# Kernel tuning notes

Measured on AMD Instinct MI355X. Metric: run time of the kernel, lower is better.

The kernel has to match this reference:

```python
import jax, jax.numpy as jnp
import numpy as np

B, N, C = 64, 196, 768
H = 12
HD = C // H            # 64
TOPK = int(0.25 * HD)  # 16
HIDDEN = int(C * 4.0)  # 3072
SCALE = HD ** -0.5
EPS = 1e-5


def layernorm(x, g, b):
    mu = jnp.mean(x, axis=-1, keepdims=True)
    var = jnp.var(x, axis=-1, keepdims=True)
    return (x - mu) * jax.lax.rsqrt(var + EPS) * g + b


def setup_inputs() -> dict:
    key = jax.random.key(0)
    ks = jax.random.split(key, 8)
    s = 0.02
    return {
        "x": jax.random.normal(ks[0], (B, N, C), jnp.float32),
        "norm1_g": jnp.ones((C,), jnp.float32),
        "norm1_b": jnp.zeros((C,), jnp.float32),
        "qk_w": jax.random.normal(ks[1], (2 * C, C), jnp.float32) * s,   # torch Linear [out,in], no bias
        "attn_proj_w": jax.random.normal(ks[2], (C, H * TOPK), jnp.float32) * s,
        "attn_proj_b": jnp.zeros((C,), jnp.float32),
        "norm2_g": jnp.ones((C,), jnp.float32),
        "norm2_b": jnp.zeros((C,), jnp.float32),
        "fc1_w": jax.random.normal(ks[3], (HIDDEN, C), jnp.float32) * s,
        "fc1_b": jnp.zeros((HIDDEN,), jnp.float32),
        "fc2_w": jax.random.normal(ks[4], (C, HIDDEN), jnp.float32) * s,
        "fc2_b": jnp.zeros((C,), jnp.float32),
    }


def reference(x, norm1_g, norm1_b, qk_w, attn_proj_w, attn_proj_b,
              norm2_g, norm2_b, fc1_w, fc1_b, fc2_w, fc2_b):
    # --- HomoAttention branch ---
    h = layernorm(x, norm1_g, norm1_b)                       # [B,N,C]
    qk = h @ qk_w.T                                          # [B,N,2C]
    qk = qk.reshape(B, N, 2, H, HD).transpose(2, 0, 3, 1, 4) # [2,B,H,N,HD]
    q, k = qk[0] * SCALE, qk[1]
    attn = jnp.einsum('bhnd,bhmd->bhnm', q, k)               # [B,H,N,N]
    top_vals, _ = jax.lax.top_k(attn, TOPK)                  # [B,H,N,TOPK]
    a = jax.nn.softmax(top_vals, axis=-1)
    a = a.transpose(0, 2, 1, 3).reshape(B, N, H * TOPK)      # [B,N,H*TOPK]
    x = x + a @ attn_proj_w.T + attn_proj_b

    # --- MLP branch ---
    h2 = layernorm(x, norm2_g, norm2_b)
    h2 = jax.nn.gelu(h2 @ fc1_w.T + fc1_b, approximate=False)
    x = x + h2 @ fc2_w.T + fc2_b
    return x
```

## Files before the change

### kernel.cpp

```cpp
#include <hip/hip_runtime.h>


#define BATCH 64
#define SEQ   196
#define CH    768
#define NHEAD 12
#define HDIM  64
#define TOPK  16
#define HID   3072
#define MROWS 12544
#define MHALF 6272
#define SCALE_F 0.125f
#define NEGBIG -3e38f

typedef __bf16 bf16x8 __attribute__((ext_vector_type(8)));
typedef float  f32x4  __attribute__((ext_vector_type(4)));

__device__ __forceinline__ unsigned short f2b(float f) {
    union { float f; unsigned int i; } c; c.f = f;
    unsigned int u = c.i;
    return (unsigned short)((u + 0x7fffu + ((u >> 16) & 1u)) >> 16);
}

__device__ __forceinline__ void async16(const unsigned short* g, unsigned short* l) {
    __builtin_amdgcn_global_load_lds(
        (const __attribute__((address_space(1))) unsigned int*)(g),
        (__attribute__((address_space(3))) unsigned int*)(l), 16, 0, 0);
}

__global__ __launch_bounds__(256) void f2b4_k(const float* __restrict__ s0, unsigned short* __restrict__ d0, int n0,
                                              const float* __restrict__ s1, unsigned short* __restrict__ d1, int n1,
                                              const float* __restrict__ s2, unsigned short* __restrict__ d2, int n2,
                                              const float* __restrict__ s3, unsigned short* __restrict__ d3, int n3)
{
    int idx = (blockIdx.x * 256 + threadIdx.x) * 4;
    const float* s; unsigned short* d; int n;
    if (idx < n0) { s = s0; d = d0; n = n0; }
    else {
        idx -= n0;
        if (idx < n1) { s = s1; d = d1; n = n1; }
        else {
            idx -= n1;
            if (idx < n2) { s = s2; d = d2; n = n2; }
            else { idx -= n2; s = s3; d = d3; n = n3; }
        }
    }
    if (idx < n) {
        float4 v = *(const float4*)(s + idx);
        ushort4 o;
        o.x = f2b(v.x); o.y = f2b(v.y); o.z = f2b(v.z); o.w = f2b(v.w);
        *(ushort4*)(d + idx) = o;
    }
}

__global__ __launch_bounds__(256) void ln_k(const float* __restrict__ x,
                                            const float* __restrict__ gw,
                                            const float* __restrict__ bw,
                                            unsigned short* __restrict__ out)
{
    const int row = blockIdx.x;
    const int tid = threadIdx.x;
    const float* xr = x + (size_t)row * CH;
    float v0 = xr[tid], v1 = xr[tid + 256], v2 = xr[tid + 512];
    float s  = v0 + v1 + v2;
    float sq = v0*v0 + v1*v1 + v2*v2;
#pragma unroll
    for (int off = 32; off > 0; off >>= 1) {
        s  += __shfl_down(s, off, 64);
        sq += __shfl_down(sq, off, 64);
    }
    __shared__ __align__(16) float red[8];
    if ((tid & 63) == 0) { red[(tid >> 6) * 2] = s; red[(tid >> 6) * 2 + 1] = sq; }
    __syncthreads();
    s  = red[0] + red[2] + red[4] + red[6];
    sq = red[1] + red[3] + red[5] + red[7];
    float mu  = s * (1.0f / CH);
    float var = sq * (1.0f / CH) - mu * mu;
    float rs  = rsqrtf(var + 1e-5f);
    unsigned short* orow = out + (size_t)row * CH;
    orow[tid]       = f2b((v0 - mu) * rs * gw[tid]       + bw[tid]);
    orow[tid + 256] = f2b((v1 - mu) * rs * gw[tid + 256] + bw[tid + 256]);
    orow[tid + 512] = f2b((v2 - mu) * rs * gw[tid + 512] + bw[tid + 512]);
}

template<int TM, int TN, bool BIAS, bool RES, bool GELU, bool OUTF>
__global__ __launch_bounds__(256, 4)
void gemm_bt(const unsigned short* __restrict__ A,
             const unsigned short* __restrict__ Bw,
             const float* __restrict__ bias,
             const float* __restrict__ resid,
             void* __restrict__ Cout,
             int M, int N, int K)
{
    constexpr int WROWS = (TM == 128) ? 2 : 1;
    constexpr int WCOLS = 4 / WROWS;
    constexpr int JF = TN / (16 * WCOLS);
    __shared__ __align__(16) unsigned short As[2][TM * 32];
    __shared__ __align__(16) unsigned short Bs[2][TN * 32];
    const int tid  = threadIdx.x;
    const int w    = tid >> 6;
    const int lane = tid & 63;

    const int gridN = gridDim.x, gridM = gridDim.y;
    const int lid = blockIdx.y * gridN + blockIdx.x;
    const int SG = 8 * gridN;
    const int sg = lid / SG, r = lid % SG;
    const int remM = gridM - sg * 8;
    int mloc, nloc;
    if (remM >= 8) { mloc = sg * 8 + (r & 7); nloc = r >> 3; }
    else           { mloc = sg * 8 + r % remM; nloc = r / remM; }
    const int tileM = mloc * TM;
    const int tileN = nloc * TN;

    const int wm = (w / WCOLS) * 64;
    const int wn = (w % WCOLS) * (JF * 16);
    const int q   = lane >> 4;
    const int l16 = lane & 15;
    const int csw = (q ^ (l16 & 3)) * 8;

    f32x4 acc[4][JF];
#pragma unroll
    for (int i = 0; i < 4; ++i)
#pragma unroll
        for (int j = 0; j < JF; ++j) acc[i][j] = (f32x4){0.f, 0.f, 0.f, 0.f};

    const int r0 = tid >> 2;
    const int g0 = ((tid & 3) ^ (r0 & 3)) * 8;

    const int kIters = K >> 5;

    auto stage = [&](int kt, int buf) {
        const size_t koff = (size_t)kt * 32 + g0;
#pragma unroll
        for (int c = 0; c < TN / 64; ++c)
            async16(Bw + (size_t)(tileN + r0 + c * 64) * K + koff,
                    &Bs[buf][(size_t)(c * 256 + w * 64) * 8]);
#pragma unroll
        for (int c = 0; c < TM / 64; ++c)
            async16(A + (size_t)(tileM + r0 + c * 64) * K + koff,
                    &As[buf][(size_t)(c * 256 + w * 64) * 8]);
    };

    stage(0, 0);
    int cur = 0;
    for (int kt = 0; kt < kIters; ++kt) {
        __syncthreads();
        if (kt + 1 < kIters) stage(kt + 1, cur ^ 1);
        bf16x8 af[4], bfr[JF];
#pragma unroll
        for (int i = 0; i < 4; ++i)
            af[i] = *(const bf16x8*)&As[cur][(wm + i * 16 + l16) * 32 + csw];
#pragma unroll
        for (int j = 0; j < JF; ++j)
            bfr[j] = *(const bf16x8*)&Bs[cur][(wn + j * 16 + l16) * 32 + csw];
#pragma unroll
        for (int i = 0; i < 4; ++i)
#pragma unroll
            for (int j = 0; j < JF; ++j)
                acc[i][j] = __builtin_amdgcn_mfma_f32_16x16x32_bf16(af[i], bfr[j], acc[i][j], 0, 0, 0);
        cur ^= 1;
    }

#pragma unroll
    for (int i = 0; i < 4; ++i) {
#pragma unroll
        for (int r2 = 0; r2 < 4; ++r2) {
            int row = tileM + wm + i * 16 + q * 4 + r2;
#pragma unroll
            for (int j = 0; j < JF; ++j) {
                int col = tileN + wn + j * 16 + l16;
                float v = acc[i][j][r2];
                if (BIAS) v += bias[col];
                if (GELU) v = 0.5f * v * (1.0f + erff(v * 0.70710678118f));
                if (RES)  v += resid[(size_t)row * N + col];
                if (OUTF) ((float*)Cout)[(size_t)row * N + col] = v;
                else      ((unsigned short*)Cout)[(size_t)row * N + col] = f2b(v);
            }
        }
    }
}

__global__ __launch_bounds__(256) void attn_topk(const unsigned short* __restrict__ qk,
                                                 unsigned short* __restrict__ aout)
{
    const int bh = blockIdx.x;
    const int b = bh / NHEAD, h = bh % NHEAD;
    __shared__ __align__(16) unsigned short Qs[208 * 64];
    __shared__ __align__(16) unsigned short Ks[208 * 64];
    const int tid = threadIdx.x;

    for (int i = tid; i < 208 * 8; i += 256) {
        int row = i >> 3, c = i & 7;
        uint4 vq = make_uint4(0, 0, 0, 0), vk = vq;
        if (row < SEQ) {
            const uint4* gp = (const uint4*)(qk + ((size_t)(b * SEQ + row) * 1536 + h * 64));
            vq = gp[c];
            vk = gp[c + 96];
        }
        int slot = c ^ (row & 7);
        *(uint4*)&Qs[row * 64 + slot * 8] = vq;
        *(uint4*)&Ks[row * 64 + slot * 8] = vk;
    }
    __syncthreads();

    const int w = tid >> 6, lane = tid & 63;
    const int q = lane >> 4, l16 = lane & 15;

    for (int tn = w; tn < 13; tn += 4) {
        const int nrow = tn * 16 + l16;
        const int nsw = nrow & 7;
        bf16x8 bq0 = *(const bf16x8*)&Qs[nrow * 64 + ((0 * 4 + q) ^ nsw) * 8];
        bf16x8 bq1 = *(const bf16x8*)&Qs[nrow * 64 + ((1 * 4 + q) ^ nsw) * 8];

        float t[TOPK];
#pragma unroll
        for (int j = 0; j < TOPK; ++j) t[j] = NEGBIG;

        for (int tm = 0; tm < 12; ++tm) {
            const int mrow = tm * 16 + l16;
            const int msw = mrow & 7;
            bf16x8 ak0 = *(const bf16x8*)&Ks[mrow * 64 + ((0 * 4 + q) ^ msw) * 8];
            bf16x8 ak1 = *(const bf16x8*)&Ks[mrow * 64 + ((1 * 4 + q) ^ msw) * 8];
            f32x4 acc = (f32x4){0.f, 0.f, 0.f, 0.f};
            acc = __builtin_amdgcn_mfma_f32_16x16x32_bf16(ak0, bq0, acc, 0, 0, 0);
            acc = __builtin_amdgcn_mfma_f32_16x16x32_bf16(ak1, bq1, acc, 0, 0, 0);
#pragma unroll
            for (int r = 0; r < 4; ++r) {
                float v = acc[r];
#pragma unroll
                for (int j = 0; j < TOPK; ++j) {
                    float mx = fmaxf(t[j], v);
                    v = fminf(t[j], v);
                    t[j] = mx;
                }
            }
        }
        {
            const int mrow = 12 * 16 + l16;
            const int msw = mrow & 7;
            bf16x8 ak0 = *(const bf16x8*)&Ks[mrow * 64 + ((0 * 4 + q) ^ msw) * 8];
            bf16x8 ak1 = *(const bf16x8*)&Ks[mrow * 64 + ((1 * 4 + q) ^ msw) * 8];
            f32x4 acc = (f32x4){0.f, 0.f, 0.f, 0.f};
            acc = __builtin_amdgcn_mfma_f32_16x16x32_bf16(ak0, bq0, acc, 0, 0, 0);
            acc = __builtin_amdgcn_mfma_f32_16x16x32_bf16(ak1, bq1, acc, 0, 0, 0);
#pragma unroll
            for (int r = 0; r < 4; ++r) {
                float v = (q == 0) ? acc[r] : NEGBIG;
#pragma unroll
                for (int j = 0; j < TOPK; ++j) {
                    float mx = fmaxf(t[j], v);
                    v = fminf(t[j], v);
                    t[j] = mx;
                }
            }
        }

#pragma unroll
        for (int stage = 0; stage < 2; ++stage) {
            const int xm = 16 << stage;
            float bl[TOPK], c[TOPK];
#pragma unroll
            for (int j = 0; j < TOPK; ++j) bl[j] = __shfl_xor(t[j], xm, 64);
#pragma unroll
            for (int j = 0; j < TOPK; ++j) c[j] = fmaxf(t[j], bl[TOPK - 1 - j]);
#pragma unroll
            for (int s = 8; s >= 1; s >>= 1) {
#pragma unroll
                for (int i = 0; i < TOPK; ++i) {
                    if ((i & s) == 0) {
                        float mx = fmaxf(c[i], c[i + s]);
                        c[i + s] = fminf(c[i], c[i + s]);
                        c[i] = mx;
                    }
                }
            }
#pragma unroll
            for (int j = 0; j < TOPK; ++j) t[j] = c[j];
        }

        if (q == 0 && nrow < SEQ) {
            float e[TOPK], sum = 0.f;
#pragma unroll
            for (int j = 0; j < TOPK; ++j) { e[j] = __expf((t[j] - t[0]) * SCALE_F); sum += e[j]; }
            float inv = 1.0f / sum;
            unsigned int pk[8];
#pragma unroll
            for (int jj = 0; jj < 8; ++jj)
                pk[jj] = (unsigned int)f2b(e[2 * jj] * inv) |
                         ((unsigned int)f2b(e[2 * jj + 1] * inv) << 16);
            unsigned short* dst = aout + ((size_t)(b * SEQ + nrow)) * (NHEAD * TOPK) + h * TOPK;
            ((uint4*)dst)[0] = make_uint4(pk[0], pk[1], pk[2], pk[3]);
            ((uint4*)dst)[1] = make_uint4(pk[4], pk[5], pk[6], pk[7]);
        }
    }
}

extern "C" void kernel_launch(void* const* d_in, const int* in_sizes, int n_in,
                              void* d_out, int out_size, void* d_ws, size_t ws_size,
                              hipStream_t stream)
{
    const float* x    = (const float*)d_in[0];
    const float* g1   = (const float*)d_in[1];
    const float* bb1  = (const float*)d_in[2];
    const float* qkw  = (const float*)d_in[3];
    const float* pw   = (const float*)d_in[4];
    const float* pb   = (const float*)d_in[5];
    const float* g2   = (const float*)d_in[6];
    const float* bb2  = (const float*)d_in[7];
    const float* f1w  = (const float*)d_in[8];
    const float* f1b  = (const float*)d_in[9];
    const float* f2w  = (const float*)d_in[10];
    const float* f2bp = (const float*)d_in[11];
    float* out = (float*)d_out;

    char* ws = (char*)d_ws;
    const size_t SZ_H   = (size_t)MROWS * CH * 2;
    const size_t N_WQK  = (size_t)2 * CH * CH;
    const size_t N_WP   = (size_t)CH * (NHEAD * TOPK);
    const size_t N_WF   = (size_t)HID * CH;
    const size_t SZ_W   = (N_WQK + N_WP + 2 * N_WF) * 2;
    const size_t SZ_A   = (size_t)MROWS * (NHEAD * TOPK) * 2;
    const size_t SZ_GGF = (size_t)MROWS * HID * 2;

    unsigned short* hbuf = (unsigned short*)(ws);
    unsigned short* wqk  = (unsigned short*)(ws + SZ_H);
    unsigned short* wp   = wqk + N_WQK;
    unsigned short* wf1  = wp  + N_WP;
    unsigned short* wf2  = wf1 + N_WF;
    unsigned short* av   = (unsigned short*)(ws + SZ_H + SZ_W);
    unsigned short* qk   = (unsigned short*)(ws + SZ_H + SZ_W + SZ_A);
    unsigned short* gg   = qk;
    float* x1 = out;

    const bool fullMLP = ws_size >= SZ_H + SZ_W + SZ_A + SZ_GGF;

    {
        int total4 = (int)((N_WQK + N_WP + 2 * N_WF) / 4);
        f2b4_k<<<(total4 + 255) / 256, 256, 0, stream>>>(
            qkw, wqk, (int)N_WQK, pw, wp, (int)N_WP,
            f1w, wf1, (int)N_WF, f2w, wf2, (int)N_WF);
    }

    ln_k<<<MROWS, 256, 0, stream>>>(x, g1, bb1, hbuf);
    gemm_bt<128, 128, false, false, false, false><<<dim3(12, 98), 256, 0, stream>>>(
        hbuf, wqk, nullptr, nullptr, qk, MROWS, 2*CH, CH);
    attn_topk<<<BATCH * NHEAD, 256, 0, stream>>>(qk, av);
    gemm_bt<64, 128, true, true, false, true><<<dim3(6, 196), 256, 0, stream>>>(
        av, wp, pb, x, x1, MROWS, CH, NHEAD*TOPK);
    ln_k<<<MROWS, 256, 0, stream>>>(x1, g2, bb2, hbuf);

    if (fullMLP) {
        gemm_bt<128, 128, true, false, true, false><<<dim3(24, 98), 256, 0, stream>>>(
            hbuf, wf1, f1b, nullptr, gg, MROWS, HID, CH);
        gemm_bt<64, 256, true, true, false, true><<<dim3(3, 196), 256, 0, stream>>>(
            gg, wf2, f2bp, x1, out, MROWS, CH, HID);
    } else {
        for (int half = 0; half < 2; ++half) {
            const size_t ro = (size_t)half * MHALF;
            gemm_bt<128, 128, true, false, true, false><<<dim3(24, 49), 256, 0, stream>>>(
                hbuf + ro * CH, wf1, f1b, nullptr, gg, MHALF, HID, CH);
            gemm_bt<64, 256, true, true, false, true><<<dim3(3, 98), 256, 0, stream>>>(
                gg, wf2, f2bp, x1 + ro * CH, out + ro * CH, MHALF, CH, HID);
        }
    }
}
```

Baseline: 439.3 us.

## Use tanh GELU, bf16 intermediate residual, and incremental staging pointers

```diff
diff --git a/kernel.cpp b/kernel.cpp
--- a/kernel.cpp
+++ b/kernel.cpp
@@ -20,6 +20,16 @@
     union { float f; unsigned int i; } c; c.f = f;
     unsigned int u = c.i;
     return (unsigned short)((u + 0x7fffu + ((u >> 16) & 1u)) >> 16);
+}
+__device__ __forceinline__ float b2f(unsigned short u) {
+    union { unsigned int i; float f; } c; c.i = ((unsigned int)u) << 16; return c.f;
+}
+
+__device__ __forceinline__ float gelu_f(float v) {
+    float u = v * (0.7978845608f + 0.0356774081f * v * v);
+    float e = __expf(2.0f * u);
+    float th = 1.0f - 2.0f / (e + 1.0f);
+    return 0.5f * v * (1.0f + th);
 }
 
 __device__ __forceinline__ void async16(const unsigned short* g, unsigned short* l) {
@@ -53,15 +63,22 @@
     }
 }
 
-__global__ __launch_bounds__(256) void ln_k(const float* __restrict__ x,
+template<bool INF32>
+__global__ __launch_bounds__(256) void ln_k(const void* __restrict__ xin,
                                             const float* __restrict__ gw,
                                             const float* __restrict__ bw,
                                             unsigned short* __restrict__ out)
 {
     const int row = blockIdx.x;
     const int tid = threadIdx.x;
-    const float* xr = x + (size_t)row * CH;
-    float v0 = xr[tid], v1 = xr[tid + 256], v2 = xr[tid + 512];
+    float v0, v1, v2;
+    if constexpr (INF32) {
+        const float* xr = (const float*)xin + (size_t)row * CH;
+        v0 = xr[tid]; v1 = xr[tid + 256]; v2 = xr[tid + 512];
+    } else {
+        const unsigned short* xr = (const unsigned short*)xin + (size_t)row * CH;
+        v0 = b2f(xr[tid]); v1 = b2f(xr[tid + 256]); v2 = b2f(xr[tid + 512]);
+    }
     float s  = v0 + v1 + v2;
     float sq = v0*v0 + v1*v1 + v2*v2;
 #pragma unroll
@@ -83,12 +100,12 @@
     orow[tid + 512] = f2b((v2 - mu) * rs * gw[tid + 512] + bw[tid + 512]);
 }
 
-template<int TM, int TN, bool BIAS, bool RES, bool GELU, bool OUTF>
+template<int TM, int TN, bool BIAS, int RES, bool GELU, bool OUTF>
 __global__ __launch_bounds__(256, 4)
 void gemm_bt(const unsigned short* __restrict__ A,
              const unsigned short* __restrict__ Bw,
              const float* __restrict__ bias,
-             const float* __restrict__ resid,
+             const void* __restrict__ resid,
              void* __restrict__ Cout,
              int M, int N, int K)
 {
@@ -127,25 +144,32 @@
     const int r0 = tid >> 2;
     const int g0 = ((tid & 3) ^ (r0 & 3)) * 8;
 
+    const unsigned short* pB[TN / 64];
+    const unsigned short* pA[TM / 64];
+#pragma unroll
+    for (int c = 0; c < TN / 64; ++c) pB[c] = Bw + (size_t)(tileN + r0 + c * 64) * K + g0;
+#pragma unroll
+    for (int c = 0; c < TM / 64; ++c) pA[c] = A + (size_t)(tileM + r0 + c * 64) * K + g0;
+
+    auto stage = [&](int buf) {
+#pragma unroll
+        for (int c = 0; c < TN / 64; ++c) {
+            async16(pB[c], &Bs[buf][(size_t)(c * 256 + w * 64) * 8]);
+            pB[c] += 32;
+        }
+#pragma unroll
+        for (int c = 0; c < TM / 64; ++c) {
+            async16(pA[c], &As[buf][(size_t)(c * 256 + w * 64) * 8]);
+            pA[c] += 32;
+        }
+    };
+
     const int kIters = K >> 5;
-
-    auto stage = [&](int kt, int buf) {
-        const size_t koff = (size_t)kt * 32 + g0;
-#pragma unroll
-        for (int c = 0; c < TN / 64; ++c)
-            async16(Bw + (size_t)(tileN + r0 + c * 64) * K + koff,
-                    &Bs[buf][(size_t)(c * 256 + w * 64) * 8]);
-#pragma unroll
-        for (int c = 0; c < TM / 64; ++c)
-            async16(A + (size_t)(tileM + r0 + c * 64) * K + koff,
-                    &As[buf][(size_t)(c * 256 + w * 64) * 8]);
-    };
-
-    stage(0, 0);
+    stage(0);
     int cur = 0;
     for (int kt = 0; kt < kIters; ++kt) {
         __syncthreads();
-        if (kt + 1 < kIters) stage(kt + 1, cur ^ 1);
+        if (kt + 1 < kIters) stage(cur ^ 1);
         bf16x8 af[4], bfr[JF];
 #pragma unroll
         for (int i = 0; i < 4; ++i)
@@ -171,8 +195,9 @@
                 int col = tileN + wn + j * 16 + l16;
                 float v = acc[i][j][r2];
                 if (BIAS) v += bias[col];
-                if (GELU) v = 0.5f * v * (1.0f + erff(v * 0.70710678118f));
-                if (RES)  v += resid[(size_t)row * N + col];
+                if (GELU) v = gelu_f(v);
+                if (RES == 1) v += ((const float*)resid)[(size_t)row * N + col];
+                if (RES == 2) v += b2f(((const unsigned short*)resid)[(size_t)row * N + col]);
                 if (OUTF) ((float*)Cout)[(size_t)row * N + col] = v;
                 else      ((unsigned short*)Cout)[(size_t)row * N + col] = f2b(v);
             }
@@ -320,6 +345,7 @@
     const size_t N_WF   = (size_t)HID * CH;
     const size_t SZ_W   = (N_WQK + N_WP + 2 * N_WF) * 2;
     const size_t SZ_A   = (size_t)MROWS * (NHEAD * TOPK) * 2;
+    const size_t SZ_QK  = (size_t)MROWS * 2 * CH * 2;
     const size_t SZ_GGF = (size_t)MROWS * HID * 2;
 
     unsigned short* hbuf = (unsigned short*)(ws);
@@ -330,9 +356,12 @@
     unsigned short* av   = (unsigned short*)(ws + SZ_H + SZ_W);
     unsigned short* qk   = (unsigned short*)(ws + SZ_H + SZ_W + SZ_A);
     unsigned short* gg   = qk;
+
+    const size_t base = SZ_H + SZ_W + SZ_A;
+    const bool fullMLP = ws_size >= base + SZ_GGF + SZ_H;
+    const bool bx1     = fullMLP || ws_size >= base + SZ_QK + SZ_H;
+    unsigned short* x1b = (unsigned short*)(ws + base + (fullMLP ? SZ_GGF : SZ_QK));
     float* x1 = out;
-
-    const bool fullMLP = ws_size >= SZ_H + SZ_W + SZ_A + SZ_GGF;
 
     {
         int total4 = (int)((N_WQK + N_WP + 2 * N_WF) / 4);
@@ -341,25 +370,38 @@
             f1w, wf1, (int)N_WF, f2w, wf2, (int)N_WF);
     }
 
-    ln_k<<<MROWS, 256, 0, stream>>>(x, g1, bb1, hbuf);
-    gemm_bt<128, 128, false, false, false, false><<<dim3(12, 98), 256, 0, stream>>>(
+    ln_k<true><<<MROWS, 256, 0, stream>>>(x, g1, bb1, hbuf);
+    gemm_bt<128, 128, false, 0, false, false><<<dim3(12, 98), 256, 0, stream>>>(
         hbuf, wqk, nullptr, nullptr, qk, MROWS, 2*CH, CH);
     attn_topk<<<BATCH * NHEAD, 256, 0, stream>>>(qk, av);
-    gemm_bt<64, 128, true, true, false, true><<<dim3(6, 196), 256, 0, stream>>>(
-        av, wp, pb, x, x1, MROWS, CH, NHEAD*TOPK);
-    ln_k<<<MROWS, 256, 0, stream>>>(x1, g2, bb2, hbuf);
-
-    if (fullMLP) {
-        gemm_bt<128, 128, true, false, true, false><<<dim3(24, 98), 256, 0, stream>>>(
-            hbuf, wf1, f1b, nullptr, gg, MROWS, HID, CH);
-        gemm_bt<64, 256, true, true, false, true><<<dim3(3, 196), 256, 0, stream>>>(
-            gg, wf2, f2bp, x1, out, MROWS, CH, HID);
+
+    if (bx1) {
+        gemm_bt<64, 128, true, 1, false, false><<<dim3(6, 196), 256, 0, stream>>>(
+            av, wp, pb, x, x1b, MROWS, CH, NHEAD*TOPK);
+        ln_k<false><<<MROWS, 256, 0, stream>>>(x1b, g2, bb2, hbuf);
+        if (fullMLP) {
+            gemm_bt<128, 128, true, 0, true, false><<<dim3(24, 98), 256, 0, stream>>>(
+                hbuf, wf1, f1b, nullptr, gg, MROWS, HID, CH);
+            gemm_bt<64, 256, true, 2, false, true><<<dim3(3, 196), 256, 0, stream>>>(
+                gg, wf2, f2bp, x1b, out, MROWS, CH, HID);
+        } else {
+            for (int half = 0; half < 2; ++half) {
+                const size_t ro = (size_t)half * MHALF;
+                gemm_bt<128, 128, true, 0, true, false><<<dim3(24, 49), 256, 0, stream>>>(
+                    hbuf + ro * CH, wf1, f1b, nullptr, gg, MHALF, HID, CH);
+                gemm_bt<64, 256, true, 2, false, true><<<dim3(3, 98), 256, 0, stream>>>(
+                    gg, wf2, f2bp, x1b + ro * CH, out + ro * CH, MHALF, CH, HID);
+            }
+        }
     } else {
+        gemm_bt<64, 128, true, 1, false, true><<<dim3(6, 196), 256, 0, stream>>>(
+            av, wp, pb, x, x1, MROWS, CH, NHEAD*TOPK);
+        ln_k<true><<<MROWS, 256, 0, stream>>>(x1, g2, bb2, hbuf);
         for (int half = 0; half < 2; ++half) {
             const size_t ro = (size_t)half * MHALF;
-            gemm_bt<128, 128, true, false, true, false><<<dim3(24, 49), 256, 0, stream>>>(
+            gemm_bt<128, 128, true, 0, true, false><<<dim3(24, 49), 256, 0, stream>>>(
                 hbuf + ro * CH, wf1, f1b, nullptr, gg, MHALF, HID, CH);
-            gemm_bt<64, 256, true, true, false, true><<<dim3(3, 98), 256, 0, stream>>>(
+            gemm_bt<64, 256, true, 1, false, true><<<dim3(3, 98), 256, 0, stream>>>(
                 gg, wf2, f2bp, x1 + ro * CH, out + ro * CH, MHALF, CH, HID);
         }
     }
```

Result: no change. 433.5 us (-1.3%).
